# Performance work log

Hardware: AMD Instinct MI355X
Metric: run time of the kernel (lower is better)

The kernel has to match this reference:

```python
import jax, jax.numpy as jnp
import numpy as np

B, K, SD, NA = 2, 512, 60, 5
E, H, D, FF, NL = 256, 4, 64, 1024, 2
EPS_F = 1e-6   # feature_eps in phi(x)=relu(x)+eps
LN_EPS = 1e-5  # torch LayerNorm default eps


def setup_inputs() -> dict:
    key = jax.random.key(0)
    ks = jax.random.split(key, 16)
    f = lambda i, shape, s=0.02: jax.random.normal(ks[i], shape, dtype=jnp.float32) * s
    return {
        "rtg": jax.random.normal(ks[0], (B, K, 1), dtype=jnp.float32),
        "state": jax.random.normal(ks[1], (B, K, SD), dtype=jnp.float32),
        "action": jax.random.normal(ks[2], (B, K, NA), dtype=jnp.float32),
        "rtg_w": f(3, (1, E)), "rtg_b": jnp.zeros((E,), jnp.float32),
        "state_w": f(4, (SD, E)), "state_b": jnp.zeros((E,), jnp.float32),
        "action_w": f(5, (NA, E)), "action_b": jnp.zeros((E,), jnp.float32),
        "pos_emb": f(6, (K, E)),
        "norm1_g": jnp.ones((NL, E), jnp.float32), "norm1_b": jnp.zeros((NL, E), jnp.float32),
        "qkv_w": f(7, (NL, E, 3 * E)), "qkv_b": jnp.zeros((NL, 3 * E), jnp.float32),
        "out_w": f(8, (NL, E, E)), "out_b": jnp.zeros((NL, E), jnp.float32),
        "norm2_g": jnp.ones((NL, E), jnp.float32), "norm2_b": jnp.zeros((NL, E), jnp.float32),
        "ffn1_w": f(9, (NL, E, FF)), "ffn1_b": jnp.zeros((NL, FF), jnp.float32),
        "ffn2_w": f(10, (NL, FF, E)), "ffn2_b": jnp.zeros((NL, E), jnp.float32),
        "normf_g": jnp.ones((E,), jnp.float32), "normf_b": jnp.zeros((E,), jnp.float32),
        "pred_w": f(11, (E, NA)), "pred_b": jnp.zeros((NA,), jnp.float32),
    }


def _ln(x, g, b):
    m = x.mean(-1, keepdims=True)
    v = jnp.mean((x - m) ** 2, -1, keepdims=True)
    return (x - m) * jax.lax.rsqrt(v + LN_EPS) * g + b


def _attn(x, qkv_w, qkv_b, out_w, out_b):
    b, l, _ = x.shape
    qkv = (x @ qkv_w + qkv_b).reshape(b, l, 3, H, D).transpose(2, 0, 3, 1, 4)
    q, k, v = qkv[0], qkv[1], qkv[2]          # each (b,h,l,d)
    q = jax.nn.relu(q) + EPS_F
    k = jax.nn.relu(k) + EPS_F
    kv = jnp.cumsum(jnp.einsum('bhld,bhle->bhlde', k, v), axis=2)  # (b,h,l,d,e)
    kcum = jnp.cumsum(k, axis=2)
    num = jnp.einsum('bhld,bhlde->bhle', q, kv)
    den = jnp.maximum(jnp.einsum('bhld,bhld->bhl', q, kcum)[..., None], 1e-6)
    o = (num / den).transpose(0, 2, 1, 3).reshape(b, l, H * D)
    return o @ out_w + out_b


def reference(rtg, state, action, rtg_w, rtg_b, state_w, state_b, action_w, action_b,
              pos_emb, norm1_g, norm1_b, qkv_w, qkv_b, out_w, out_b,
              norm2_g, norm2_b, ffn1_w, ffn1_b, ffn2_w, ffn2_b,
              normf_g, normf_b, pred_w, pred_b):
    b, k, _ = state.shape
    p = pos_emb[:k][None]
    r = rtg @ rtg_w + rtg_b + p
    s = state @ state_w + state_b + p
    a = action @ action_w + action_b + p
    # interleave (r,s,a) per timestep -> (b, 3k, E)
    x = jnp.stack((r, s, a), axis=2).reshape(b, 3 * k, E)
    for i in range(NL):
        x = x + _attn(_ln(x, norm1_g[i], norm1_b[i]), qkv_w[i], qkv_b[i], out_w[i], out_b[i])
        h = _ln(x, norm2_g[i], norm2_b[i])
        h = jax.nn.gelu(h @ ffn1_w[i] + ffn1_b[i], approximate=False) @ ffn2_w[i] + ffn2_b[i]
        x = x + h
    x = _ln(x, normf_g, normf_b)
    return x[:, 1::3, :] @ pred_w + pred_b  # predict from state tokens -> (b,k,num_actions)
```

## Files before the change

kernel.cpp:

```cpp
#include <hip/hip_runtime.h>
#include <hip/hip_bf16.h>
#include <math.h>

#define B_  2
#define K_  512
#define SD_ 60
#define NA_ 5
#define E_  256
#define H_  4
#define D_  64
#define FF_ 1024
#define NL_ 2
#define L_  (3 * K_)
#define M_  (B_ * L_)
#define EPS_F 1e-6f
#define LN_EPS 1e-5f
#define CHK 64
#define NC_ (L_ / CHK)

using bf16x8 = __attribute__((ext_vector_type(8))) short;
using f32x4  = __attribute__((ext_vector_type(4))) float;
typedef unsigned short u16;

__device__ inline u16 f2b(float v) {
    __hip_bfloat16 h = __float2bfloat16(v);
    return *(u16*)&h;
}
__device__ inline float b2f(u16 v) {
    __hip_bfloat16 h = *(__hip_bfloat16*)&v;
    return __bfloat162float(h);
}

__global__ __launch_bounds__(256) void init_kernel(
    const float* __restrict__ qkv_w, const float* __restrict__ out_w,
    const float* __restrict__ ffn1_w, const float* __restrict__ ffn2_w,
    u16* __restrict__ qkvT, u16* __restrict__ outT,
    u16* __restrict__ f1T, u16* __restrict__ f2T,
    const float* __restrict__ rtg, const float* __restrict__ state,
    const float* __restrict__ action,
    const float* __restrict__ rtg_w, const float* __restrict__ rtg_b,
    const float* __restrict__ state_w, const float* __restrict__ state_b,
    const float* __restrict__ action_w, const float* __restrict__ action_b,
    const float* __restrict__ pos,
    const float* __restrict__ g, const float* __restrict__ bta,
    float* __restrict__ X, u16* __restrict__ Y)
{
    __shared__ u16 T[32][33];
    if (blockIdx.x < 1536) {
        int tb = blockIdx.x;
        int layer = tb / 768;
        int r = tb % 768;
        const float* src; u16* dst; int K, N, tidx;
        if (r < 192)      { src = qkv_w  + layer * 196608; dst = qkvT + layer * 196608; K = 256;  N = 768;  tidx = r; }
        else if (r < 256) { src = out_w  + layer * 65536;  dst = outT + layer * 65536;  K = 256;  N = 256;  tidx = r - 192; }
        else if (r < 512) { src = ffn1_w + layer * 262144; dst = f1T  + layer * 262144; K = 256;  N = 1024; tidx = r - 256; }
        else              { src = ffn2_w + layer * 262144; dst = f2T  + layer * 262144; K = 1024; N = 256;  tidx = r - 512; }
        int tilesN = N >> 5;
        int k0 = (tidx / tilesN) << 5;
        int n0 = (tidx % tilesN) << 5;
        int c = threadIdx.x & 31, r0 = threadIdx.x >> 5;
        for (int rr = r0; rr < 32; rr += 8)
            T[rr][c] = f2b(src[(size_t)(k0 + rr) * N + n0 + c]);
        __syncthreads();
        for (int rr = r0; rr < 32; rr += 8)
            dst[(size_t)(n0 + rr) * K + k0 + c] = T[c][rr];
        return;
    }
    int tok = (blockIdx.x - 1536) * 4 + (threadIdx.x >> 6);
    int lane = threadIdx.x & 63;
    int b = tok / L_, l = tok % L_;
    int j = l % 3, t = l / 3;
    int e0 = lane * 4;
    float4 val = *(const float4*)(pos + t * E_ + e0);
    if (j == 0) {
        float rv = rtg[b * K_ + t];
        float4 w = *(const float4*)(rtg_w + e0);
        float4 bb = *(const float4*)(rtg_b + e0);
        val.x += rv * w.x + bb.x; val.y += rv * w.y + bb.y;
        val.z += rv * w.z + bb.z; val.w += rv * w.w + bb.w;
    } else if (j == 1) {
        float4 a = *(const float4*)(state_b + e0);
        const float* srow = state + ((size_t)b * K_ + t) * SD_;
        for (int i = 0; i < SD_; i++) {
            float s = srow[i];
            float4 w = *(const float4*)(state_w + (size_t)i * E_ + e0);
            a.x += s * w.x; a.y += s * w.y; a.z += s * w.z; a.w += s * w.w;
        }
        val.x += a.x; val.y += a.y; val.z += a.z; val.w += a.w;
    } else {
        float4 a = *(const float4*)(action_b + e0);
        const float* arow = action + ((size_t)b * K_ + t) * NA_;
        #pragma unroll
        for (int i = 0; i < NA_; i++) {
            float s = arow[i];
            float4 w = *(const float4*)(action_w + (size_t)i * E_ + e0);
            a.x += s * w.x; a.y += s * w.y; a.z += s * w.z; a.w += s * w.w;
        }
        val.x += a.x; val.y += a.y; val.z += a.z; val.w += a.w;
    }
    *(float4*)(X + (size_t)tok * E_ + e0) = val;
    float s = val.x + val.y + val.z + val.w;
    #pragma unroll
    for (int o = 32; o; o >>= 1) s += __shfl_xor(s, o, 64);
    float mean = s * (1.f / E_);
    float dx = val.x - mean, dy = val.y - mean, dz = val.z - mean, dw = val.w - mean;
    float q = dx * dx + dy * dy + dz * dz + dw * dw;
    #pragma unroll
    for (int o = 32; o; o >>= 1) q += __shfl_xor(q, o, 64);
    float inv = rsqrtf(q * (1.f / E_) + LN_EPS);
    float4 gv = *(const float4*)(g + e0);
    float4 bv = *(const float4*)(bta + e0);
    ushort4 u;
    u.x = f2b(dx * inv * gv.x + bv.x); u.y = f2b(dy * inv * gv.y + bv.y);
    u.z = f2b(dz * inv * gv.z + bv.z); u.w = f2b(dw * inv * gv.w + bv.w);
    *(ushort4*)(Y + (size_t)tok * E_ + e0) = u;
}

template <int EPI>
__global__ __launch_bounds__(256) void mgemm64(
    const u16* __restrict__ A, const u16* __restrict__ Bt,
    const float* __restrict__ bias,
    u16* __restrict__ C, int M, int N, int Kd)
{
    __shared__ __align__(16) u16 As[2][64 * 40];
    __shared__ __align__(16) u16 Bs[2][128 * 40];
    int tid = threadIdx.x;
    int bm = blockIdx.y * 64, bn = blockIdx.x * 128;
    int wave = tid >> 6, lane = tid & 63;
    int wm = (wave >> 1) * 32, wn = (wave & 1) * 64;
    int lr = lane & 15, kg = lane >> 4;

    int r0 = tid >> 2, g0 = (tid & 3) * 8;

    const u16* Ap  = A  + (size_t)(bm + r0) * Kd + g0;
    const u16* Bp0 = Bt + (size_t)(bn + r0) * Kd + g0;
    const u16* Bp1 = Bt + (size_t)(bn + r0 + 64) * Kd + g0;

    uint4 a0 = *(const uint4*)(Ap);
    uint4 b0 = *(const uint4*)(Bp0);
    uint4 b1 = *(const uint4*)(Bp1);
    *(uint4*)&As[0][r0 * 40 + g0] = a0;
    *(uint4*)&Bs[0][r0 * 40 + g0] = b0;
    *(uint4*)&Bs[0][(r0 + 64) * 40 + g0] = b1;

    f32x4 acc[2][4] = {};
    int NT = Kd >> 5;
    for (int t = 0; t < NT; ++t) {
        int cur = t & 1;
        __syncthreads();
        if (t + 1 < NT) {
            int k1 = (t + 1) << 5;
            a0 = *(const uint4*)(Ap + k1);
            b0 = *(const uint4*)(Bp0 + k1);
            b1 = *(const uint4*)(Bp1 + k1);
        }
        bf16x8 af[2], bg[4];
        #pragma unroll
        for (int i = 0; i < 2; i++)
            af[i] = *(const bf16x8*)&As[cur][(wm + i * 16 + lr) * 40 + kg * 8];
        #pragma unroll
        for (int j = 0; j < 4; j++)
            bg[j] = *(const bf16x8*)&Bs[cur][(wn + j * 16 + lr) * 40 + kg * 8];
        #pragma unroll
        for (int i = 0; i < 2; i++)
            #pragma unroll
            for (int j = 0; j < 4; j++)
                acc[i][j] = __builtin_amdgcn_mfma_f32_16x16x32_bf16(
                    af[i], bg[j], acc[i][j], 0, 0, 0);
        if (t + 1 < NT) {
            *(uint4*)&As[cur ^ 1][r0 * 40 + g0] = a0;
            *(uint4*)&Bs[cur ^ 1][r0 * 40 + g0] = b0;
            *(uint4*)&Bs[cur ^ 1][(r0 + 64) * 40 + g0] = b1;
        }
    }

    #pragma unroll
    for (int i = 0; i < 2; i++) {
        #pragma unroll
        for (int j = 0; j < 4; j++) {
            int col = bn + wn + j * 16 + lr;
            float bc = bias[col];
            #pragma unroll
            for (int r = 0; r < 4; r++) {
                int row = bm + wm + i * 16 + kg * 4 + r;
                float v = acc[i][j][r] + bc;
                if (EPI == 1) v = 0.5f * v * (1.0f + erff(v * 0.70710678118654752f));
                if (EPI == 2) { if (col < 512) v = fmaxf(v, 0.f) + EPS_F; }
                C[(size_t)row * N + col] = f2b(v);
            }
        }
    }
}

template <int LNOUT>
__global__ __launch_bounds__(512) void gres_ln(
    const u16* __restrict__ A, const u16* __restrict__ Bt,
    const float* __restrict__ bias, float* __restrict__ X,
    const float* __restrict__ g, const float* __restrict__ bt,
    u16* __restrict__ Y, int Kd)
{
    __shared__ __align__(16) char smem[5120 + 40960];
    u16* AsB = (u16*)smem;
    u16* BsB = (u16*)(smem + 5120);
    int tid = threadIdx.x;
    int bm = blockIdx.x * 32;
    int wave = tid >> 6, lane = tid & 63;
    int wm = (wave >> 2) * 16;
    int wn = (wave & 3) * 64;
    int lr = lane & 15, kg = lane >> 4;

    int ar = tid >> 2, ag = (tid & 3) * 8;
    bool aload = ar < 32;

    const u16* Ap  = A  + (size_t)(bm + ar) * Kd + ag;
    const u16* Bp0 = Bt + (size_t)(ar) * Kd + ag;
    const u16* Bp1 = Bt + (size_t)(ar + 128) * Kd + ag;

    uint4 a0, b0, b1;
    if (aload) a0 = *(const uint4*)(Ap);
    b0 = *(const uint4*)(Bp0);
    b1 = *(const uint4*)(Bp1);
    if (aload) *(uint4*)&AsB[ar * 40 + ag] = a0;
    *(uint4*)&BsB[ar * 40 + ag] = b0;
    *(uint4*)&BsB[(ar + 128) * 40 + ag] = b1;

    f32x4 acc[4] = {};
    int NT = Kd >> 5;
    for (int t = 0; t < NT; ++t) {
        int cur = t & 1;
        __syncthreads();
        if (t + 1 < NT) {
            int k1 = (t + 1) << 5;
            if (aload) a0 = *(const uint4*)(Ap + k1);
            b0 = *(const uint4*)(Bp0 + k1);
            b1 = *(const uint4*)(Bp1 + k1);
        }
        bf16x8 af = *(const bf16x8*)&AsB[cur * 1280 + (wm + lr) * 40 + kg * 8];
        bf16x8 bg[4];
        #pragma unroll
        for (int j = 0; j < 4; j++)
            bg[j] = *(const bf16x8*)&BsB[cur * 10240 + (wn + j * 16 + lr) * 40 + kg * 8];
        #pragma unroll
        for (int j = 0; j < 4; j++)
            acc[j] = __builtin_amdgcn_mfma_f32_16x16x32_bf16(af, bg[j], acc[j], 0, 0, 0);
        if (t + 1 < NT) {
            if (aload) *(uint4*)&AsB[(cur ^ 1) * 1280 + ar * 40 + ag] = a0;
            *(uint4*)&BsB[(cur ^ 1) * 10240 + ar * 40 + ag] = b0;
            *(uint4*)&BsB[(cur ^ 1) * 10240 + (ar + 128) * 40 + ag] = b1;
        }
    }
    __syncthreads();

    float* Xs = (float*)smem;
    #pragma unroll
    for (int j = 0; j < 4; j++) {
        int col = wn + j * 16 + lr;
        float bc = bias[col];
        #pragma unroll
        for (int rr = 0; rr < 4; rr++) {
            int row = wm + kg * 4 + rr;
            float v = acc[j][rr] + bc + X[(size_t)(bm + row) * 256 + col];
            Xs[row * 260 + col] = v;
        }
    }
    __syncthreads();

    int e0 = lane * 4;
    #pragma unroll
    for (int rq = 0; rq < 4; rq++) {
        int row = wave * 4 + rq;
        float4 v = *(const float4*)&Xs[row * 260 + e0];
        *(float4*)(X + (size_t)(bm + row) * 256 + e0) = v;
        if (LNOUT) {
            float s = v.x + v.y + v.z + v.w;
            #pragma unroll
            for (int o = 32; o; o >>= 1) s += __shfl_xor(s, o, 64);
            float mean = s * (1.f / E_);
            float dx = v.x - mean, dy = v.y - mean, dz = v.z - mean, dw = v.w - mean;
            float q = dx * dx + dy * dy + dz * dz + dw * dw;
            #pragma unroll
            for (int o = 32; o; o >>= 1) q += __shfl_xor(q, o, 64);
            float inv = rsqrtf(q * (1.f / E_) + LN_EPS);
            float4 gv = *(const float4*)(g + e0);
            float4 bv = *(const float4*)(bt + e0);
            ushort4 u;
            u.x = f2b(dx * inv * gv.x + bv.x); u.y = f2b(dy * inv * gv.y + bv.y);
            u.z = f2b(dz * inv * gv.z + bv.z); u.w = f2b(dw * inv * gv.w + bv.w);
            *(ushort4*)(Y + (size_t)(bm + row) * 256 + e0) = u;
        }
    }
}

__global__ __launch_bounds__(256) void chunk_sum_kernel(
    const u16* __restrict__ QKV, float* __restrict__ S, float* __restrict__ Z)
{
    int blk = blockIdx.x;
    int c = blk % NC_;
    int bh = blk / NC_;
    int h = bh % H_;
    int b = bh / H_;
    __shared__ __align__(16) u16 Kt[64 * 72];
    __shared__ __align__(16) u16 Vt[64 * 72];
    int tid = threadIdx.x;
    const size_t base = ((size_t)b * L_ + (size_t)c * CHK) * 768 + h * 64;
    for (int i = tid; i < 1024; i += 256) {
        int t = i >> 4, d4 = (i & 15) << 2;
        ushort4 k = *(const ushort4*)(QKV + base + (size_t)t * 768 + 256 + d4);
        ushort4 v = *(const ushort4*)(QKV + base + (size_t)t * 768 + 512 + d4);
        Kt[(d4 + 0) * 72 + t] = k.x;
        Kt[(d4 + 1) * 72 + t] = k.y;
        Kt[(d4 + 2) * 72 + t] = k.z;
        Kt[(d4 + 3) * 72 + t] = k.w;
        Vt[(d4 + 0) * 72 + t] = v.x;
        Vt[(d4 + 1) * 72 + t] = v.y;
        Vt[(d4 + 2) * 72 + t] = v.z;
        Vt[(d4 + 3) * 72 + t] = v.w;
    }
    __syncthreads();
    int wave = tid >> 6, lane = tid & 63;
    int lr = lane & 15, kg = lane >> 4;
    int wm = wave * 16;
    bf16x8 a0 = *(const bf16x8*)&Kt[(wm + lr) * 72 + kg * 8];
    bf16x8 a1 = *(const bf16x8*)&Kt[(wm + lr) * 72 + 32 + kg * 8];
    f32x4 acc[4] = {};
    #pragma unroll
    for (int j = 0; j < 4; j++) {
        bf16x8 b0 = *(const bf16x8*)&Vt[(j * 16 + lr) * 72 + kg * 8];
        bf16x8 b1 = *(const bf16x8*)&Vt[(j * 16 + lr) * 72 + 32 + kg * 8];
        acc[j] = __builtin_amdgcn_mfma_f32_16x16x32_bf16(a0, b0, acc[j], 0, 0, 0);
        acc[j] = __builtin_amdgcn_mfma_f32_16x16x32_bf16(a1, b1, acc[j], 0, 0, 0);
    }
    if (tid < 64) {
        float z = 0.f;
        #pragma unroll 8
        for (int t = 0; t < 64; t++) z += b2f(Kt[tid * 72 + t]);
        Z[(size_t)blk * 64 + tid] = z;
    }
    float* Sp = S + (size_t)blk * 4096;
    #pragma unroll
    for (int j = 0; j < 4; j++) {
        #pragma unroll
        for (int rr = 0; rr < 4; rr++) {
            int d = wm + kg * 4 + rr;
            int e = j * 16 + lr;
            Sp[d * 64 + e] = acc[j][rr];
        }
    }
}

__global__ __launch_bounds__(256) void chunk_out_kernel(
    const u16* __restrict__ QKV, const float* __restrict__ S,
    const float* __restrict__ Z, u16* __restrict__ O)
{
    int blk = blockIdx.x;
    int c = blk % NC_;
    int bh = blk / NC_;
    int h = bh % H_;
    int b = bh / H_;
    __shared__ __align__(16) u16 Qb[64 * 72];
    __shared__ __align__(16) u16 Kb[64 * 72];
    __shared__ __align__(16) u16 Vt[64 * 72];
    __shared__ __align__(16) u16 KVt[64 * 72];
    __shared__ __align__(16) u16 Ps[64 * 72];
    __shared__ float kzs[64];
    __shared__ float rows[64];
    __shared__ float invs[64];
    int tid = threadIdx.x;
    const size_t base = ((size_t)b * L_ + (size_t)c * CHK) * 768 + h * 64;
    const float* Sbh = S + (size_t)bh * NC_ * 4096;
    for (int i = tid; i < 1024; i += 256) {
        int t = i >> 4, d4 = (i & 15) << 2;
        ushort4 q = *(const ushort4*)(QKV + base + (size_t)t * 768 + d4);
        ushort4 k = *(const ushort4*)(QKV + base + (size_t)t * 768 + 256 + d4);
        ushort4 v = *(const ushort4*)(QKV + base + (size_t)t * 768 + 512 + d4);
        *(ushort4*)&Qb[t * 72 + d4] = q;
        *(ushort4*)&Kb[t * 72 + d4] = k;
        Vt[(d4 + 0) * 72 + t] = v.x;
        Vt[(d4 + 1) * 72 + t] = v.y;
        Vt[(d4 + 2) * 72 + t] = v.z;
        Vt[(d4 + 3) * 72 + t] = v.w;
        int d = t, e4 = d4;
        float4 a = make_float4(0.f, 0.f, 0.f, 0.f);
        for (int cc = 0; cc < c; cc++) {
            float4 s4 = *(const float4*)(Sbh + (size_t)cc * 4096 + d * 64 + e4);
            a.x += s4.x; a.y += s4.y; a.z += s4.z; a.w += s4.w;
        }
        KVt[(e4 + 0) * 72 + d] = f2b(a.x);
        KVt[(e4 + 1) * 72 + d] = f2b(a.y);
        KVt[(e4 + 2) * 72 + d] = f2b(a.z);
        KVt[(e4 + 3) * 72 + d] = f2b(a.w);
    }
    if (tid < 64) {
        float z = 0.f;
        const float* Zbh = Z + (size_t)bh * NC_ * 64;
        for (int cc = 0; cc < c; cc++) z += Zbh[cc * 64 + tid];
        kzs[tid] = z;
    }
    __syncthreads();

    int wave = tid >> 6, lane = tid & 63;
    int lr = lane & 15, kg = lane >> 4;
    int wm = wave * 16;

    bf16x8 aq0 = *(const bf16x8*)&Qb[(wm + lr) * 72 + kg * 8];
    bf16x8 aq1 = *(const bf16x8*)&Qb[(wm + lr) * 72 + 32 + kg * 8];

    f32x4 accs[4] = {};
    #pragma unroll
    for (int j = 0; j < 4; j++) {
        bf16x8 b0 = *(const bf16x8*)&Kb[(j * 16 + lr) * 72 + kg * 8];
        bf16x8 b1 = *(const bf16x8*)&Kb[(j * 16 + lr) * 72 + 32 + kg * 8];
        accs[j] = __builtin_amdgcn_mfma_f32_16x16x32_bf16(aq0, b0, accs[j], 0, 0, 0);
        accs[j] = __builtin_amdgcn_mfma_f32_16x16x32_bf16(aq1, b1, accs[j], 0, 0, 0);
    }
    float rsum[4] = {0.f, 0.f, 0.f, 0.f};
    #pragma unroll
    for (int j = 0; j < 4; j++) {
        #pragma unroll
        for (int rr = 0; rr < 4; rr++) {
            int m = wm + kg * 4 + rr;
            int n = j * 16 + lr;
            float v = (n <= m) ? accs[j][rr] : 0.f;
            rsum[rr] += v;
            Ps[m * 72 + n] = f2b(v);
        }
    }
    #pragma unroll
    for (int rr = 0; rr < 4; rr++) {
        float s = rsum[rr];
        s += __shfl_xor(s, 1, 64);
        s += __shfl_xor(s, 2, 64);
        s += __shfl_xor(s, 4, 64);
        s += __shfl_xor(s, 8, 64);
        if (lr == 0) rows[wm + kg * 4 + rr] = s;
    }
    __syncthreads();

    if (tid < 64) {
        float den = rows[tid];
        float acc = 0.f;
        #pragma unroll 8
        for (int d = 0; d < 64; d++) acc += b2f(Qb[tid * 72 + d]) * kzs[d];
        invs[tid] = 1.f / fmaxf(den + acc, 1e-6f);
    }

    bf16x8 ap0 = *(const bf16x8*)&Ps[(wm + lr) * 72 + kg * 8];
    bf16x8 ap1 = *(const bf16x8*)&Ps[(wm + lr) * 72 + 32 + kg * 8];
    f32x4 accn[4] = {};
    #pragma unroll
    for (int j = 0; j < 4; j++) {
        bf16x8 b0 = *(const bf16x8*)&KVt[(j * 16 + lr) * 72 + kg * 8];
        bf16x8 b1 = *(const bf16x8*)&KVt[(j * 16 + lr) * 72 + 32 + kg * 8];
        accn[j] = __builtin_amdgcn_mfma_f32_16x16x32_bf16(aq0, b0, accn[j], 0, 0, 0);
        accn[j] = __builtin_amdgcn_mfma_f32_16x16x32_bf16(aq1, b1, accn[j], 0, 0, 0);
        bf16x8 c0 = *(const bf16x8*)&Vt[(j * 16 + lr) * 72 + kg * 8];
        bf16x8 c1 = *(const bf16x8*)&Vt[(j * 16 + lr) * 72 + 32 + kg * 8];
        accn[j] = __builtin_amdgcn_mfma_f32_16x16x32_bf16(ap0, c0, accn[j], 0, 0, 0);
        accn[j] = __builtin_amdgcn_mfma_f32_16x16x32_bf16(ap1, c1, accn[j], 0, 0, 0);
    }
    __syncthreads();

    u16* Op = O + ((size_t)b * L_ + (size_t)c * CHK) * E_ + h * 64;
    #pragma unroll
    for (int j = 0; j < 4; j++) {
        #pragma unroll
        for (int rr = 0; rr < 4; rr++) {
            int m = wm + kg * 4 + rr;
            int e = j * 16 + lr;
            Op[(size_t)m * E_ + e] = f2b(accn[j][rr] * invs[m]);
        }
    }
}

__global__ __launch_bounds__(256) void lnpred_kernel(
    const float* __restrict__ X, const float* __restrict__ g,
    const float* __restrict__ bt, const float* __restrict__ W,
    const float* __restrict__ bias, float* __restrict__ Out)
{
    int si = blockIdx.x * 4 + (threadIdx.x >> 6);
    int lane = threadIdx.x & 63;
    int b = si / K_, t = si % K_;
    size_t row = (size_t)b * L_ + 3 * t + 1;
    int e0 = lane * 4;
    float4 v = *(const float4*)(X + row * E_ + e0);
    float s = v.x + v.y + v.z + v.w;
    #pragma unroll
    for (int o = 32; o; o >>= 1) s += __shfl_xor(s, o, 64);
    float mean = s * (1.f / E_);
    float dx = v.x - mean, dy = v.y - mean, dz = v.z - mean, dw = v.w - mean;
    float q = dx * dx + dy * dy + dz * dz + dw * dw;
    #pragma unroll
    for (int o = 32; o; o >>= 1) q += __shfl_xor(q, o, 64);
    float inv = rsqrtf(q * (1.f / E_) + LN_EPS);
    float4 gv = *(const float4*)(g + e0);
    float4 bv = *(const float4*)(bt + e0);
    float y0 = dx * inv * gv.x + bv.x;
    float y1 = dy * inv * gv.y + bv.y;
    float y2 = dz * inv * gv.z + bv.z;
    float y3 = dw * inv * gv.w + bv.w;
    #pragma unroll
    for (int na = 0; na < NA_; na++) {
        float a = y0 * W[(e0 + 0) * NA_ + na] + y1 * W[(e0 + 1) * NA_ + na]
                + y2 * W[(e0 + 2) * NA_ + na] + y3 * W[(e0 + 3) * NA_ + na];
        #pragma unroll
        for (int o = 32; o; o >>= 1) a += __shfl_xor(a, o, 64);
        if (lane == 0) Out[(size_t)si * NA_ + na] = a + bias[na];
    }
}

extern "C" void kernel_launch(void* const* d_in, const int* in_sizes, int n_in,
                              void* d_out, int out_size, void* d_ws, size_t ws_size,
                              hipStream_t stream) {
    const float* rtg      = (const float*)d_in[0];
    const float* state    = (const float*)d_in[1];
    const float* action   = (const float*)d_in[2];
    const float* rtg_w    = (const float*)d_in[3];
    const float* rtg_b    = (const float*)d_in[4];
    const float* state_w  = (const float*)d_in[5];
    const float* state_b  = (const float*)d_in[6];
    const float* action_w = (const float*)d_in[7];
    const float* action_b = (const float*)d_in[8];
    const float* pos_emb  = (const float*)d_in[9];
    const float* norm1_g  = (const float*)d_in[10];
    const float* norm1_b  = (const float*)d_in[11];
    const float* qkv_w    = (const float*)d_in[12];
    const float* qkv_b    = (const float*)d_in[13];
    const float* out_w    = (const float*)d_in[14];
    const float* out_b    = (const float*)d_in[15];
    const float* norm2_g  = (const float*)d_in[16];
    const float* norm2_b  = (const float*)d_in[17];
    const float* ffn1_w   = (const float*)d_in[18];
    const float* ffn1_b   = (const float*)d_in[19];
    const float* ffn2_w   = (const float*)d_in[20];
    const float* ffn2_b   = (const float*)d_in[21];
    const float* normf_g  = (const float*)d_in[22];
    const float* normf_b  = (const float*)d_in[23];
    const float* pred_w   = (const float*)d_in[24];
    const float* pred_b   = (const float*)d_in[25];
    float* out = (float*)d_out;

    float* ws = (float*)d_ws;
    float* x    = ws;
    float* S    = x + 786432;
    float* Z    = S + 786432;
    u16*   yb   = (u16*)(Z + 12288);
    u16*   qkvb = yb + 786432;
    u16*   att  = qkvb + 2359296;
    u16*   h1   = att + 786432;
    u16*   qkvT = h1 + 3145728;
    u16*   outT = qkvT + 393216;
    u16*   f1T  = outT + 131072;
    u16*   f2T  = f1T + 524288;

    init_kernel<<<2304, 256, 0, stream>>>(
        qkv_w, out_w, ffn1_w, ffn2_w, qkvT, outT, f1T, f2T,
        rtg, state, action, rtg_w, rtg_b, state_w, state_b,
        action_w, action_b, pos_emb, norm1_g, norm1_b, x, yb);

    for (int i = 0; i < NL_; i++) {
        mgemm64<2><<<dim3(768 / 128, M_ / 64), 256, 0, stream>>>(
            yb, qkvT + (size_t)i * 196608, qkv_b + i * 768, qkvb,
            M_, 768, E_);
        chunk_sum_kernel<<<B_ * H_ * NC_, 256, 0, stream>>>(qkvb, S, Z);
        chunk_out_kernel<<<B_ * H_ * NC_, 256, 0, stream>>>(qkvb, S, Z, att);
        gres_ln<1><<<M_ / 32, 512, 0, stream>>>(
            att, outT + (size_t)i * 65536, out_b + i * E_, x,
            norm2_g + i * E_, norm2_b + i * E_, yb, E_);
        mgemm64<1><<<dim3(FF_ / 128, M_ / 64), 256, 0, stream>>>(
            yb, f1T + (size_t)i * 262144, ffn1_b + i * FF_, h1,
            M_, FF_, E_);
        if (i == 0)
            gres_ln<1><<<M_ / 32, 512, 0, stream>>>(
                h1, f2T + (size_t)i * 262144, ffn2_b + i * E_, x,
                norm1_g + E_, norm1_b + E_, yb, FF_);
        else
            gres_ln<0><<<M_ / 32, 512, 0, stream>>>(
                h1, f2T + (size_t)i * 262144, ffn2_b + i * E_, x,
                normf_g, normf_b, yb, FF_);
    }
    lnpred_kernel<<<(B_ * K_) / 4, 256, 0, stream>>>(
        x, normf_g, normf_b, pred_w, pred_b, out);
}
```

Measured before the change: 262.5 us.

## Fuse all stages into one persistent kernel with atomic grid barriers

Replaces the sequence of separate kernel launches with a single persistent kernel of 224 blocks. Stages are separated by a software grid barrier built on an atomic counter, and work items are handed out per block in strided loops. It also switches the GEMM tile from 64x128 to 128x128, folds the final LayerNorm and prediction head into the last residual GEMM, and runs the residual GEMM with 256 threads over 32-row tiles. The aim is to remove launch overhead and inter-kernel gaps. The cost is fewer, larger tiles, lower occupancy, and barrier spin time, and the barrier relies on all 224 blocks being resident at once.

```diff
diff --git a/kernel.cpp b/kernel.cpp
--- a/kernel.cpp
+++ b/kernel.cpp
@@ -17,6 +17,7 @@
 #define LN_EPS 1e-5f
 #define CHK 64
 #define NC_ (L_ / CHK)
+#define NBLK 224
 
 using bf16x8 = __attribute__((ext_vector_type(8))) short;
 using f32x4  = __attribute__((ext_vector_type(4))) float;
@@ -31,74 +32,83 @@
     return __bfloat162float(h);
 }
 
-__global__ __launch_bounds__(256) void init_kernel(
-    const float* __restrict__ qkv_w, const float* __restrict__ out_w,
-    const float* __restrict__ ffn1_w, const float* __restrict__ ffn2_w,
-    u16* __restrict__ qkvT, u16* __restrict__ outT,
-    u16* __restrict__ f1T, u16* __restrict__ f2T,
-    const float* __restrict__ rtg, const float* __restrict__ state,
-    const float* __restrict__ action,
-    const float* __restrict__ rtg_w, const float* __restrict__ rtg_b,
-    const float* __restrict__ state_w, const float* __restrict__ state_b,
-    const float* __restrict__ action_w, const float* __restrict__ action_b,
-    const float* __restrict__ pos,
-    const float* __restrict__ g, const float* __restrict__ bta,
-    float* __restrict__ X, u16* __restrict__ Y)
-{
-    __shared__ u16 T[32][33];
-    if (blockIdx.x < 1536) {
-        int tb = blockIdx.x;
-        int layer = tb / 768;
-        int r = tb % 768;
-        const float* src; u16* dst; int K, N, tidx;
-        if (r < 192)      { src = qkv_w  + layer * 196608; dst = qkvT + layer * 196608; K = 256;  N = 768;  tidx = r; }
-        else if (r < 256) { src = out_w  + layer * 65536;  dst = outT + layer * 65536;  K = 256;  N = 256;  tidx = r - 192; }
-        else if (r < 512) { src = ffn1_w + layer * 262144; dst = f1T  + layer * 262144; K = 256;  N = 1024; tidx = r - 256; }
-        else              { src = ffn2_w + layer * 262144; dst = f2T  + layer * 262144; K = 1024; N = 256;  tidx = r - 512; }
-        int tilesN = N >> 5;
-        int k0 = (tidx / tilesN) << 5;
-        int n0 = (tidx % tilesN) << 5;
-        int c = threadIdx.x & 31, r0 = threadIdx.x >> 5;
-        for (int rr = r0; rr < 32; rr += 8)
-            T[rr][c] = f2b(src[(size_t)(k0 + rr) * N + n0 + c]);
-        __syncthreads();
-        for (int rr = r0; rr < 32; rr += 8)
-            dst[(size_t)(n0 + rr) * K + k0 + c] = T[c][rr];
-        return;
-    }
-    int tok = (blockIdx.x - 1536) * 4 + (threadIdx.x >> 6);
+struct MP {
+    const float *rtg, *state, *action, *rtg_w, *rtg_b, *state_w, *state_b,
+                *action_w, *action_b, *pos;
+    const float *n1g, *n1b, *qkv_b, *out_b, *n2g, *n2b, *f1b, *ffn2b,
+                *nfg, *nfb, *pw, *pb;
+    const float *qkv_w, *out_w, *f1w, *f2w;
+    float *x, *S, *Z, *out;
+    u16 *yb, *qkvb, *att, *h1, *qkvT, *outT, *f1T, *f2T;
+    unsigned *bar;
+};
+
+__device__ inline void gbar(unsigned* c) {
+    __syncthreads();
+    if (threadIdx.x == 0) {
+        __threadfence();
+        unsigned t = atomicAdd(c, 1u);
+        unsigned target = (t / gridDim.x + 1u) * gridDim.x;
+        while (atomicAdd(c, 0u) < target) __builtin_amdgcn_s_sleep(2);
+        __threadfence();
+    }
+    __syncthreads();
+}
+
+__device__ void dev_transpose(int tb, const MP& p, char* sm) {
+    u16 (*T)[33] = (u16(*)[33])sm;
+    int layer = tb / 768;
+    int r = tb % 768;
+    const float* src; u16* dst; int K, N, tidx;
+    if (r < 192)      { src = p.qkv_w + layer * 196608; dst = p.qkvT + layer * 196608; K = 256;  N = 768;  tidx = r; }
+    else if (r < 256) { src = p.out_w + layer * 65536;  dst = p.outT + layer * 65536;  K = 256;  N = 256;  tidx = r - 192; }
+    else if (r < 512) { src = p.f1w + layer * 262144;   dst = p.f1T  + layer * 262144; K = 256;  N = 1024; tidx = r - 256; }
+    else              { src = p.f2w + layer * 262144;   dst = p.f2T  + layer * 262144; K = 1024; N = 256;  tidx = r - 512; }
+    int tilesN = N >> 5;
+    int k0 = (tidx / tilesN) << 5;
+    int n0 = (tidx % tilesN) << 5;
+    int c = threadIdx.x & 31, r0 = threadIdx.x >> 5;
+    for (int rr = r0; rr < 32; rr += 8)
+        T[rr][c] = f2b(src[(size_t)(k0 + rr) * N + n0 + c]);
+    __syncthreads();
+    for (int rr = r0; rr < 32; rr += 8)
+        dst[(size_t)(n0 + rr) * K + k0 + c] = T[c][rr];
+}
+
+__device__ void dev_embed(int idx, const MP& p) {
+    int tok = idx * 4 + (threadIdx.x >> 6);
     int lane = threadIdx.x & 63;
     int b = tok / L_, l = tok % L_;
     int j = l % 3, t = l / 3;
     int e0 = lane * 4;
-    float4 val = *(const float4*)(pos + t * E_ + e0);
+    float4 val = *(const float4*)(p.pos + t * E_ + e0);
     if (j == 0) {
-        float rv = rtg[b * K_ + t];
-        float4 w = *(const float4*)(rtg_w + e0);
-        float4 bb = *(const float4*)(rtg_b + e0);
+        float rv = p.rtg[b * K_ + t];
+        float4 w = *(const float4*)(p.rtg_w + e0);
+        float4 bb = *(const float4*)(p.rtg_b + e0);
         val.x += rv * w.x + bb.x; val.y += rv * w.y + bb.y;
         val.z += rv * w.z + bb.z; val.w += rv * w.w + bb.w;
     } else if (j == 1) {
-        float4 a = *(const float4*)(state_b + e0);
-        const float* srow = state + ((size_t)b * K_ + t) * SD_;
+        float4 a = *(const float4*)(p.state_b + e0);
+        const float* srow = p.state + ((size_t)b * K_ + t) * SD_;
         for (int i = 0; i < SD_; i++) {
             float s = srow[i];
-            float4 w = *(const float4*)(state_w + (size_t)i * E_ + e0);
+            float4 w = *(const float4*)(p.state_w + (size_t)i * E_ + e0);
             a.x += s * w.x; a.y += s * w.y; a.z += s * w.z; a.w += s * w.w;
         }
         val.x += a.x; val.y += a.y; val.z += a.z; val.w += a.w;
     } else {
-        float4 a = *(const float4*)(action_b + e0);
-        const float* arow = action + ((size_t)b * K_ + t) * NA_;
+        float4 a = *(const float4*)(p.action_b + e0);
+        const float* arow = p.action + ((size_t)b * K_ + t) * NA_;
         #pragma unroll
         for (int i = 0; i < NA_; i++) {
             float s = arow[i];
-            float4 w = *(const float4*)(action_w + (size_t)i * E_ + e0);
+            float4 w = *(const float4*)(p.action_w + (size_t)i * E_ + e0);
             a.x += s * w.x; a.y += s * w.y; a.z += s * w.z; a.w += s * w.w;
         }
         val.x += a.x; val.y += a.y; val.z += a.z; val.w += a.w;
     }
-    *(float4*)(X + (size_t)tok * E_ + e0) = val;
+    *(float4*)(p.x + (size_t)tok * E_ + e0) = val;
     float s = val.x + val.y + val.z + val.w;
     #pragma unroll
     for (int o = 32; o; o >>= 1) s += __shfl_xor(s, o, 64);
@@ -108,74 +118,82 @@
     #pragma unroll
     for (int o = 32; o; o >>= 1) q += __shfl_xor(q, o, 64);
     float inv = rsqrtf(q * (1.f / E_) + LN_EPS);
-    float4 gv = *(const float4*)(g + e0);
-    float4 bv = *(const float4*)(bta + e0);
+    float4 gv = *(const float4*)(p.n1g + e0);
+    float4 bv = *(const float4*)(p.n1b + e0);
     ushort4 u;
     u.x = f2b(dx * inv * gv.x + bv.x); u.y = f2b(dy * inv * gv.y + bv.y);
     u.z = f2b(dz * inv * gv.z + bv.z); u.w = f2b(dw * inv * gv.w + bv.w);
-    *(ushort4*)(Y + (size_t)tok * E_ + e0) = u;
+    *(ushort4*)(p.yb + (size_t)tok * E_ + e0) = u;
 }
 
 template <int EPI>
-__global__ __launch_bounds__(256) void mgemm64(
+__device__ void dev_mgemm128(
+    int task, int TN,
     const u16* __restrict__ A, const u16* __restrict__ Bt,
-    const float* __restrict__ bias,
-    u16* __restrict__ C, int M, int N, int Kd)
+    const float* __restrict__ bias, u16* __restrict__ C,
+    int N, int Kd, char* sm)
 {
-    __shared__ __align__(16) u16 As[2][64 * 40];
-    __shared__ __align__(16) u16 Bs[2][128 * 40];
+    u16* As = (u16*)sm;
+    u16* Bs = (u16*)(sm + 20480);
     int tid = threadIdx.x;
-    int bm = blockIdx.y * 64, bn = blockIdx.x * 128;
+    int bm = (task / TN) * 128, bn = (task % TN) * 128;
     int wave = tid >> 6, lane = tid & 63;
-    int wm = (wave >> 1) * 32, wn = (wave & 1) * 64;
+    int wm = (wave >> 1) * 64, wn = (wave & 1) * 64;
     int lr = lane & 15, kg = lane >> 4;
 
     int r0 = tid >> 2, g0 = (tid & 3) * 8;
-
-    const u16* Ap  = A  + (size_t)(bm + r0) * Kd + g0;
+    int r1 = r0 + 64;
+
+    const u16* Ap0 = A + (size_t)(bm + r0) * Kd + g0;
+    const u16* Ap1 = A + (size_t)(bm + r1) * Kd + g0;
     const u16* Bp0 = Bt + (size_t)(bn + r0) * Kd + g0;
-    const u16* Bp1 = Bt + (size_t)(bn + r0 + 64) * Kd + g0;
-
-    uint4 a0 = *(const uint4*)(Ap);
+    const u16* Bp1 = Bt + (size_t)(bn + r1) * Kd + g0;
+
+    uint4 a0 = *(const uint4*)(Ap0);
+    uint4 a1 = *(const uint4*)(Ap1);
     uint4 b0 = *(const uint4*)(Bp0);
     uint4 b1 = *(const uint4*)(Bp1);
-    *(uint4*)&As[0][r0 * 40 + g0] = a0;
-    *(uint4*)&Bs[0][r0 * 40 + g0] = b0;
-    *(uint4*)&Bs[0][(r0 + 64) * 40 + g0] = b1;
-
-    f32x4 acc[2][4] = {};
+    *(uint4*)&As[r0 * 40 + g0] = a0;
+    *(uint4*)&As[r1 * 40 + g0] = a1;
+    *(uint4*)&Bs[r0 * 40 + g0] = b0;
+    *(uint4*)&Bs[r1 * 40 + g0] = b1;
+
+    f32x4 acc[4][4] = {};
     int NT = Kd >> 5;
     for (int t = 0; t < NT; ++t) {
         int cur = t & 1;
         __syncthreads();
         if (t + 1 < NT) {
             int k1 = (t + 1) << 5;
-            a0 = *(const uint4*)(Ap + k1);
+            a0 = *(const uint4*)(Ap0 + k1);
+            a1 = *(const uint4*)(Ap1 + k1);
             b0 = *(const uint4*)(Bp0 + k1);
             b1 = *(const uint4*)(Bp1 + k1);
         }
-        bf16x8 af[2], bg[4];
-        #pragma unroll
-        for (int i = 0; i < 2; i++)
-            af[i] = *(const bf16x8*)&As[cur][(wm + i * 16 + lr) * 40 + kg * 8];
+        bf16x8 af[4], bg[4];
+        #pragma unroll
+        for (int i = 0; i < 4; i++)
+            af[i] = *(const bf16x8*)&As[cur * 5120 + (wm + i * 16 + lr) * 40 + kg * 8];
         #pragma unroll
         for (int j = 0; j < 4; j++)
-            bg[j] = *(const bf16x8*)&Bs[cur][(wn + j * 16 + lr) * 40 + kg * 8];
-        #pragma unroll
-        for (int i = 0; i < 2; i++)
+            bg[j] = *(const bf16x8*)&Bs[cur * 5120 + (wn + j * 16 + lr) * 40 + kg * 8];
+        #pragma unroll
+        for (int i = 0; i < 4; i++)
             #pragma unroll
             for (int j = 0; j < 4; j++)
                 acc[i][j] = __builtin_amdgcn_mfma_f32_16x16x32_bf16(
                     af[i], bg[j], acc[i][j], 0, 0, 0);
         if (t + 1 < NT) {
-            *(uint4*)&As[cur ^ 1][r0 * 40 + g0] = a0;
-            *(uint4*)&Bs[cur ^ 1][r0 * 40 + g0] = b0;
-            *(uint4*)&Bs[cur ^ 1][(r0 + 64) * 40 + g0] = b1;
-        }
-    }
-
-    #pragma unroll
-    for (int i = 0; i < 2; i++) {
+            *(uint4*)&As[(cur ^ 1) * 5120 + r0 * 40 + g0] = a0;
+            *(uint4*)&As[(cur ^ 1) * 5120 + r1 * 40 + g0] = a1;
+            *(uint4*)&Bs[(cur ^ 1) * 5120 + r0 * 40 + g0] = b0;
+            *(uint4*)&Bs[(cur ^ 1) * 5120 + r1 * 40 + g0] = b1;
+        }
+    }
+    __syncthreads();
+
+    #pragma unroll
+    for (int i = 0; i < 4; i++) {
         #pragma unroll
         for (int j = 0; j < 4; j++) {
             int col = bn + wn + j * 16 + lr;
@@ -192,115 +210,15 @@
     }
 }
 
-template <int LNOUT>
-__global__ __launch_bounds__(512) void gres_ln(
-    const u16* __restrict__ A, const u16* __restrict__ Bt,
-    const float* __restrict__ bias, float* __restrict__ X,
-    const float* __restrict__ g, const float* __restrict__ bt,
-    u16* __restrict__ Y, int Kd)
-{
-    __shared__ __align__(16) char smem[5120 + 40960];
-    u16* AsB = (u16*)smem;
-    u16* BsB = (u16*)(smem + 5120);
-    int tid = threadIdx.x;
-    int bm = blockIdx.x * 32;
-    int wave = tid >> 6, lane = tid & 63;
-    int wm = (wave >> 2) * 16;
-    int wn = (wave & 3) * 64;
-    int lr = lane & 15, kg = lane >> 4;
-
-    int ar = tid >> 2, ag = (tid & 3) * 8;
-    bool aload = ar < 32;
-
-    const u16* Ap  = A  + (size_t)(bm + ar) * Kd + ag;
-    const u16* Bp0 = Bt + (size_t)(ar) * Kd + ag;
-    const u16* Bp1 = Bt + (size_t)(ar + 128) * Kd + ag;
-
-    uint4 a0, b0, b1;
-    if (aload) a0 = *(const uint4*)(Ap);
-    b0 = *(const uint4*)(Bp0);
-    b1 = *(const uint4*)(Bp1);
-    if (aload) *(uint4*)&AsB[ar * 40 + ag] = a0;
-    *(uint4*)&BsB[ar * 40 + ag] = b0;
-    *(uint4*)&BsB[(ar + 128) * 40 + ag] = b1;
-
-    f32x4 acc[4] = {};
-    int NT = Kd >> 5;
-    for (int t = 0; t < NT; ++t) {
-        int cur = t & 1;
-        __syncthreads();
-        if (t + 1 < NT) {
-            int k1 = (t + 1) << 5;
-            if (aload) a0 = *(const uint4*)(Ap + k1);
-            b0 = *(const uint4*)(Bp0 + k1);
-            b1 = *(const uint4*)(Bp1 + k1);
-        }
-        bf16x8 af = *(const bf16x8*)&AsB[cur * 1280 + (wm + lr) * 40 + kg * 8];
-        bf16x8 bg[4];
-        #pragma unroll
-        for (int j = 0; j < 4; j++)
-            bg[j] = *(const bf16x8*)&BsB[cur * 10240 + (wn + j * 16 + lr) * 40 + kg * 8];
-        #pragma unroll
-        for (int j = 0; j < 4; j++)
-            acc[j] = __builtin_amdgcn_mfma_f32_16x16x32_bf16(af, bg[j], acc[j], 0, 0, 0);
-        if (t + 1 < NT) {
-            if (aload) *(uint4*)&AsB[(cur ^ 1) * 1280 + ar * 40 + ag] = a0;
-            *(uint4*)&BsB[(cur ^ 1) * 10240 + ar * 40 + ag] = b0;
-            *(uint4*)&BsB[(cur ^ 1) * 10240 + (ar + 128) * 40 + ag] = b1;
-        }
-    }
-    __syncthreads();
-
-    float* Xs = (float*)smem;
-    #pragma unroll
-    for (int j = 0; j < 4; j++) {
-        int col = wn + j * 16 + lr;
-        float bc = bias[col];
-        #pragma unroll
-        for (int rr = 0; rr < 4; rr++) {
-            int row = wm + kg * 4 + rr;
-            float v = acc[j][rr] + bc + X[(size_t)(bm + row) * 256 + col];
-            Xs[row * 260 + col] = v;
-        }
-    }
-    __syncthreads();
-
-    int e0 = lane * 4;
-    #pragma unroll
-    for (int rq = 0; rq < 4; rq++) {
-        int row = wave * 4 + rq;
-        float4 v = *(const float4*)&Xs[row * 260 + e0];
-        *(float4*)(X + (size_t)(bm + row) * 256 + e0) = v;
-        if (LNOUT) {
-            float s = v.x + v.y + v.z + v.w;
-            #pragma unroll
-            for (int o = 32; o; o >>= 1) s += __shfl_xor(s, o, 64);
-            float mean = s * (1.f / E_);
-            float dx = v.x - mean, dy = v.y - mean, dz = v.z - mean, dw = v.w - mean;
-            float q = dx * dx + dy * dy + dz * dz + dw * dw;
-            #pragma unroll
-            for (int o = 32; o; o >>= 1) q += __shfl_xor(q, o, 64);
-            float inv = rsqrtf(q * (1.f / E_) + LN_EPS);
-            float4 gv = *(const float4*)(g + e0);
-            float4 bv = *(const float4*)(bt + e0);
-            ushort4 u;
-            u.x = f2b(dx * inv * gv.x + bv.x); u.y = f2b(dy * inv * gv.y + bv.y);
-            u.z = f2b(dz * inv * gv.z + bv.z); u.w = f2b(dw * inv * gv.w + bv.w);
-            *(ushort4*)(Y + (size_t)(bm + row) * 256 + e0) = u;
-        }
-    }
-}
-
-__global__ __launch_bounds__(256) void chunk_sum_kernel(
-    const u16* __restrict__ QKV, float* __restrict__ S, float* __restrict__ Z)
-{
-    int blk = blockIdx.x;
+__device__ void dev_chunk_sum(int blk, const u16* __restrict__ QKV,
+                              float* __restrict__ S, float* __restrict__ Z,
+                              char* sm) {
     int c = blk % NC_;
     int bh = blk / NC_;
     int h = bh % H_;
     int b = bh / H_;
-    __shared__ __align__(16) u16 Kt[64 * 72];
-    __shared__ __align__(16) u16 Vt[64 * 72];
+    u16* Kt = (u16*)sm;
+    u16* Vt = (u16*)(sm + 9216);
     int tid = threadIdx.x;
     const size_t base = ((size_t)b * L_ + (size_t)c * CHK) * 768 + h * 64;
     for (int i = tid; i < 1024; i += 256) {
@@ -348,23 +266,22 @@
     }
 }
 
-__global__ __launch_bounds__(256) void chunk_out_kernel(
-    const u16* __restrict__ QKV, const float* __restrict__ S,
-    const float* __restrict__ Z, u16* __restrict__ O)
-{
-    int blk = blockIdx.x;
+__device__ void dev_chunk_out(int blk, const u16* __restrict__ QKV,
+                              const float* __restrict__ S,
+                              const float* __restrict__ Z,
+                              u16* __restrict__ O, char* sm) {
     int c = blk % NC_;
     int bh = blk / NC_;
     int h = bh % H_;
     int b = bh / H_;
-    __shared__ __align__(16) u16 Qb[64 * 72];
-    __shared__ __align__(16) u16 Kb[64 * 72];
-    __shared__ __align__(16) u16 Vt[64 * 72];
-    __shared__ __align__(16) u16 KVt[64 * 72];
-    __shared__ __align__(16) u16 Ps[64 * 72];
-    __shared__ float kzs[64];
-    __shared__ float rows[64];
-    __shared__ float invs[64];
+    u16* Qb  = (u16*)sm;
+    u16* Kb  = (u16*)(sm + 9216);
+    u16* Vt  = (u16*)(sm + 18432);
+    u16* KVt = (u16*)(sm + 27648);
+    u16* Ps  = (u16*)(sm + 36864);
+    float* kzs  = (float*)(sm + 46080);
+    float* rows = kzs + 64;
+    float* invs = rows + 64;
     int tid = threadIdx.x;
     const size_t base = ((size_t)b * L_ + (size_t)c * CHK) * 768 + h * 64;
     const float* Sbh = S + (size_t)bh * NC_ * 4096;
@@ -472,73 +389,206 @@
     }
 }
 
-__global__ __launch_bounds__(256) void lnpred_kernel(
-    const float* __restrict__ X, const float* __restrict__ g,
-    const float* __restrict__ bt, const float* __restrict__ W,
-    const float* __restrict__ bias, float* __restrict__ Out)
+template <int MODE>
+__device__ void dev_gres32(
+    int task, const u16* __restrict__ A, const u16* __restrict__ Bt,
+    const float* __restrict__ bias, float* __restrict__ X,
+    const float* __restrict__ g, const float* __restrict__ bt,
+    u16* __restrict__ Y, const float* __restrict__ W,
+    const float* __restrict__ pb, float* __restrict__ Out,
+    int Kd, char* sm)
 {
-    int si = blockIdx.x * 4 + (threadIdx.x >> 6);
-    int lane = threadIdx.x & 63;
-    int b = si / K_, t = si % K_;
-    size_t row = (size_t)b * L_ + 3 * t + 1;
+    u16* AsB = (u16*)sm;
+    u16* BsB = (u16*)(sm + 5120);
+    int tid = threadIdx.x;
+    int bm = task * 32;
+    int wave = tid >> 6, lane = tid & 63;
+    int wn = wave * 64;
+    int lr = lane & 15, kg = lane >> 4;
+
+    int sr = tid >> 2, ag = (tid & 3) * 8;
+    bool al = sr < 32;
+
+    const u16* Ap = A + (size_t)(bm + sr) * Kd + ag;
+    const u16* Bp = Bt + (size_t)sr * Kd + ag;
+
+    uint4 aR, bR[4];
+    if (al) aR = *(const uint4*)(Ap);
+    #pragma unroll
+    for (int q = 0; q < 4; q++) bR[q] = *(const uint4*)(Bp + (size_t)(64 * q) * Kd);
+    if (al) *(uint4*)&AsB[sr * 40 + ag] = aR;
+    #pragma unroll
+    for (int q = 0; q < 4; q++) *(uint4*)&BsB[(sr + 64 * q) * 40 + ag] = bR[q];
+
+    f32x4 acc[2][4] = {};
+    int NT = Kd >> 5;
+    for (int t = 0; t < NT; ++t) {
+        int cur = t & 1;
+        __syncthreads();
+        if (t + 1 < NT) {
+            int k1 = (t + 1) << 5;
+            if (al) aR = *(const uint4*)(Ap + k1);
+            #pragma unroll
+            for (int q = 0; q < 4; q++)
+                bR[q] = *(const uint4*)(Bp + (size_t)(64 * q) * Kd + k1);
+        }
+        bf16x8 af[2], bg[4];
+        #pragma unroll
+        for (int i = 0; i < 2; i++)
+            af[i] = *(const bf16x8*)&AsB[cur * 1280 + (i * 16 + lr) * 40 + kg * 8];
+        #pragma unroll
+        for (int j = 0; j < 4; j++)
+            bg[j] = *(const bf16x8*)&BsB[cur * 10240 + (wn + j * 16 + lr) * 40 + kg * 8];
+        #pragma unroll
+        for (int i = 0; i < 2; i++)
+            #pragma unroll
+            for (int j = 0; j < 4; j++)
+                acc[i][j] = __builtin_amdgcn_mfma_f32_16x16x32_bf16(
+                    af[i], bg[j], acc[i][j], 0, 0, 0);
+        if (t + 1 < NT) {
+            if (al) *(uint4*)&AsB[(cur ^ 1) * 1280 + sr * 40 + ag] = aR;
+            #pragma unroll
+            for (int q = 0; q < 4; q++)
+                *(uint4*)&BsB[(cur ^ 1) * 10240 + (sr + 64 * q) * 40 + ag] = bR[q];
+        }
+    }
+    __syncthreads();
+
+    float* Xs = (float*)sm;
+    #pragma unroll
+    for (int i = 0; i < 2; i++) {
+        #pragma unroll
+        for (int j = 0; j < 4; j++) {
+            int col = wn + j * 16 + lr;
+            float bc = bias[col];
+            #pragma unroll
+            for (int rr = 0; rr < 4; rr++) {
+                int row = i * 16 + kg * 4 + rr;
+                float v = acc[i][j][rr] + bc + X[(size_t)(bm + row) * 256 + col];
+                Xs[row * 260 + col] = v;
+            }
+        }
+    }
+    __syncthreads();
+
     int e0 = lane * 4;
-    float4 v = *(const float4*)(X + row * E_ + e0);
-    float s = v.x + v.y + v.z + v.w;
-    #pragma unroll
-    for (int o = 32; o; o >>= 1) s += __shfl_xor(s, o, 64);
-    float mean = s * (1.f / E_);
-    float dx = v.x - mean, dy = v.y - mean, dz = v.z - mean, dw = v.w - mean;
-    float q = dx * dx + dy * dy + dz * dz + dw * dw;
-    #pragma unroll
-    for (int o = 32; o; o >>= 1) q += __shfl_xor(q, o, 64);
-    float inv = rsqrtf(q * (1.f / E_) + LN_EPS);
-    float4 gv = *(const float4*)(g + e0);
-    float4 bv = *(const float4*)(bt + e0);
-    float y0 = dx * inv * gv.x + bv.x;
-    float y1 = dy * inv * gv.y + bv.y;
-    float y2 = dz * inv * gv.z + bv.z;
-    float y3 = dw * inv * gv.w + bv.w;
-    #pragma unroll
-    for (int na = 0; na < NA_; na++) {
-        float a = y0 * W[(e0 + 0) * NA_ + na] + y1 * W[(e0 + 1) * NA_ + na]
-                + y2 * W[(e0 + 2) * NA_ + na] + y3 * W[(e0 + 3) * NA_ + na];
-        #pragma unroll
-        for (int o = 32; o; o >>= 1) a += __shfl_xor(a, o, 64);
-        if (lane == 0) Out[(size_t)si * NA_ + na] = a + bias[na];
+    #pragma unroll
+    for (int rq = 0; rq < 8; rq++) {
+        int row = wave * 8 + rq;
+        float4 v = *(const float4*)&Xs[row * 260 + e0];
+        if (MODE == 1) {
+            *(float4*)(X + (size_t)(bm + row) * 256 + e0) = v;
+            float s = v.x + v.y + v.z + v.w;
+            #pragma unroll
+            for (int o = 32; o; o >>= 1) s += __shfl_xor(s, o, 64);
+            float mean = s * (1.f / E_);
+            float dx = v.x - mean, dy = v.y - mean, dz = v.z - mean, dw = v.w - mean;
+            float q = dx * dx + dy * dy + dz * dz + dw * dw;
+            #pragma unroll
+            for (int o = 32; o; o >>= 1) q += __shfl_xor(q, o, 64);
+            float inv = rsqrtf(q * (1.f / E_) + LN_EPS);
+            float4 gv = *(const float4*)(g + e0);
+            float4 bv = *(const float4*)(bt + e0);
+            ushort4 u;
+            u.x = f2b(dx * inv * gv.x + bv.x); u.y = f2b(dy * inv * gv.y + bv.y);
+            u.z = f2b(dz * inv * gv.z + bv.z); u.w = f2b(dw * inv * gv.w + bv.w);
+            *(ushort4*)(Y + (size_t)(bm + row) * 256 + e0) = u;
+        } else {
+            int gr = bm + row;
+            int b = gr / L_, l = gr % L_;
+            if (l % 3 == 1) {
+                float s = v.x + v.y + v.z + v.w;
+                #pragma unroll
+                for (int o = 32; o; o >>= 1) s += __shfl_xor(s, o, 64);
+                float mean = s * (1.f / E_);
+                float dx = v.x - mean, dy = v.y - mean, dz = v.z - mean, dw = v.w - mean;
+                float q = dx * dx + dy * dy + dz * dz + dw * dw;
+                #pragma unroll
+                for (int o = 32; o; o >>= 1) q += __shfl_xor(q, o, 64);
+                float inv = rsqrtf(q * (1.f / E_) + LN_EPS);
+                float4 gv = *(const float4*)(g + e0);
+                float4 bv = *(const float4*)(bt + e0);
+                float y0 = dx * inv * gv.x + bv.x;
+                float y1 = dy * inv * gv.y + bv.y;
+                float y2 = dz * inv * gv.z + bv.z;
+                float y3 = dw * inv * gv.w + bv.w;
+                int si = b * K_ + l / 3;
+                #pragma unroll
+                for (int na = 0; na < NA_; na++) {
+                    float a = y0 * W[(e0 + 0) * NA_ + na] + y1 * W[(e0 + 1) * NA_ + na]
+                            + y2 * W[(e0 + 2) * NA_ + na] + y3 * W[(e0 + 3) * NA_ + na];
+                    #pragma unroll
+                    for (int o = 32; o; o >>= 1) a += __shfl_xor(a, o, 64);
+                    if (lane == 0) Out[(size_t)si * NA_ + na] = a + pb[na];
+                }
+            }
+        }
+    }
+}
+
+__global__ __launch_bounds__(256) void mega(MP p) {
+    __shared__ __align__(16) char sm[46848];
+    int NB = gridDim.x;
+
+    for (int t = blockIdx.x; t < 2304; t += NB) {
+        if (t < 1536) dev_transpose(t, p, sm);
+        else dev_embed(t - 1536, p);
+        __syncthreads();
+    }
+    gbar(p.bar);
+
+    for (int i = 0; i < NL_; i++) {
+        for (int t = blockIdx.x; t < 144; t += NB) {
+            dev_mgemm128<2>(t, 6, p.yb, p.qkvT + (size_t)i * 196608,
+                            p.qkv_b + i * 768, p.qkvb, 768, 256, sm);
+            __syncthreads();
+        }
+        gbar(p.bar);
+        for (int t = blockIdx.x; t < 192; t += NB) {
+            dev_chunk_sum(t, p.qkvb, p.S, p.Z, sm);
+            __syncthreads();
+        }
+        gbar(p.bar);
+        for (int t = blockIdx.x; t < 192; t += NB) {
+            dev_chunk_out(t, p.qkvb, p.S, p.Z, p.att, sm);
+            __syncthreads();
+        }
+        gbar(p.bar);
+        for (int t = blockIdx.x; t < 96; t += NB) {
+            dev_gres32<1>(t, p.att, p.outT + (size_t)i * 65536, p.out_b + i * E_,
+                          p.x, p.n2g + i * E_, p.n2b + i * E_, p.yb,
+                          nullptr, nullptr, nullptr, 256, sm);
+            __syncthreads();
+        }
+        gbar(p.bar);
+        for (int t = blockIdx.x; t < 192; t += NB) {
+            dev_mgemm128<1>(t, 8, p.yb, p.f1T + (size_t)i * 262144,
+                            p.f1b + i * FF_, p.h1, 1024, 256, sm);
+            __syncthreads();
+        }
+        gbar(p.bar);
+        if (i == 0) {
+            for (int t = blockIdx.x; t < 96; t += NB) {
+                dev_gres32<1>(t, p.h1, p.f2T, p.ffn2b, p.x,
+                              p.n1g + E_, p.n1b + E_, p.yb,
+                              nullptr, nullptr, nullptr, 1024, sm);
+                __syncthreads();
+            }
+            gbar(p.bar);
+        } else {
+            for (int t = blockIdx.x; t < 96; t += NB) {
+                dev_gres32<2>(t, p.h1, p.f2T + (size_t)i * 262144, p.ffn2b + i * E_,
+                              p.x, p.nfg, p.nfb, nullptr,
+                              p.pw, p.pb, p.out, 1024, sm);
+                __syncthreads();
+            }
+        }
     }
 }
 
 extern "C" void kernel_launch(void* const* d_in, const int* in_sizes, int n_in,
                               void* d_out, int out_size, void* d_ws, size_t ws_size,
                               hipStream_t stream) {
-    const float* rtg      = (const float*)d_in[0];
-    const float* state    = (const float*)d_in[1];
-    const float* action   = (const float*)d_in[2];
-    const float* rtg_w    = (const float*)d_in[3];
-    const float* rtg_b    = (const float*)d_in[4];
-    const float* state_w  = (const float*)d_in[5];
-    const float* state_b  = (const float*)d_in[6];
-    const float* action_w = (const float*)d_in[7];
-    const float* action_b = (const float*)d_in[8];
-    const float* pos_emb  = (const float*)d_in[9];
-    const float* norm1_g  = (const float*)d_in[10];
-    const float* norm1_b  = (const float*)d_in[11];
-    const float* qkv_w    = (const float*)d_in[12];
-    const float* qkv_b    = (const float*)d_in[13];
-    const float* out_w    = (const float*)d_in[14];
-    const float* out_b    = (const float*)d_in[15];
-    const float* norm2_g  = (const float*)d_in[16];
-    const float* norm2_b  = (const float*)d_in[17];
-    const float* ffn1_w   = (const float*)d_in[18];
-    const float* ffn1_b   = (const float*)d_in[19];
-    const float* ffn2_w   = (const float*)d_in[20];
-    const float* ffn2_b   = (const float*)d_in[21];
-    const float* normf_g  = (const float*)d_in[22];
-    const float* normf_b  = (const float*)d_in[23];
-    const float* pred_w   = (const float*)d_in[24];
-    const float* pred_b   = (const float*)d_in[25];
-    float* out = (float*)d_out;
-
     float* ws = (float*)d_ws;
     float* x    = ws;
     float* S    = x + 786432;
@@ -551,33 +601,41 @@
     u16*   outT = qkvT + 393216;
     u16*   f1T  = outT + 131072;
     u16*   f2T  = f1T + 524288;
-
-    init_kernel<<<2304, 256, 0, stream>>>(
-        qkv_w, out_w, ffn1_w, ffn2_w, qkvT, outT, f1T, f2T,
-        rtg, state, action, rtg_w, rtg_b, state_w, state_b,
-        action_w, action_b, pos_emb, norm1_g, norm1_b, x, yb);
-
-    for (int i = 0; i < NL_; i++) {
-        mgemm64<2><<<dim3(768 / 128, M_ / 64), 256, 0, stream>>>(
-            yb, qkvT + (size_t)i * 196608, qkv_b + i * 768, qkvb,
-            M_, 768, E_);
-        chunk_sum_kernel<<<B_ * H_ * NC_, 256, 0, stream>>>(qkvb, S, Z);
-        chunk_out_kernel<<<B_ * H_ * NC_, 256, 0, stream>>>(qkvb, S, Z, att);
-        gres_ln<1><<<M_ / 32, 512, 0, stream>>>(
-            att, outT + (size_t)i * 65536, out_b + i * E_, x,
-            norm2_g + i * E_, norm2_b + i * E_, yb, E_);
-        mgemm64<1><<<dim3(FF_ / 128, M_ / 64), 256, 0, stream>>>(
-            yb, f1T + (size_t)i * 262144, ffn1_b + i * FF_, h1,
-            M_, FF_, E_);
-        if (i == 0)
-            gres_ln<1><<<M_ / 32, 512, 0, stream>>>(
-                h1, f2T + (size_t)i * 262144, ffn2_b + i * E_, x,
-                norm1_g + E_, norm1_b + E_, yb, FF_);
-        else
-            gres_ln<0><<<M_ / 32, 512, 0, stream>>>(
-                h1, f2T + (size_t)i * 262144, ffn2_b + i * E_, x,
-                normf_g, normf_b, yb, FF_);
-    }
-    lnpred_kernel<<<(B_ * K_) / 4, 256, 0, stream>>>(
-        x, normf_g, normf_b, pred_w, pred_b, out);
-}
+    unsigned* bar = (unsigned*)(f2T + 524288);
+
+    hipMemsetAsync(bar, 0, 64, stream);
+
+    MP p;
+    p.rtg      = (const float*)d_in[0];
+    p.state    = (const float*)d_in[1];
+    p.action   = (const float*)d_in[2];
+    p.rtg_w    = (const float*)d_in[3];
+    p.rtg_b    = (const float*)d_in[4];
+    p.state_w  = (const float*)d_in[5];
+    p.state_b  = (const float*)d_in[6];
+    p.action_w = (const float*)d_in[7];
+    p.action_b = (const float*)d_in[8];
+    p.pos      = (const float*)d_in[9];
+    p.n1g      = (const float*)d_in[10];
+    p.n1b      = (const float*)d_in[11];
+    p.qkv_w    = (const float*)d_in[12];
+    p.qkv_b    = (const float*)d_in[13];
+    p.out_w    = (const float*)d_in[14];
+    p.out_b    = (const float*)d_in[15];
+    p.n2g      = (const float*)d_in[16];
+    p.n2b      = (const float*)d_in[17];
+    p.f1w      = (const float*)d_in[18];
+    p.f1b      = (const float*)d_in[19];
+    p.f2w      = (const float*)d_in[20];
+    p.ffn2b    = (const float*)d_in[21];
+    p.nfg      = (const float*)d_in[22];
+    p.nfb      = (const float*)d_in[23];
+    p.pw       = (const float*)d_in[24];
+    p.pb       = (const float*)d_in[25];
+    p.x = x; p.S = S; p.Z = Z; p.out = (float*)d_out;
+    p.yb = yb; p.qkvb = qkvb; p.att = att; p.h1 = h1;
+    p.qkvT = qkvT; p.outT = outT; p.f1T = f1T; p.f2T = f2T;
+    p.bar = bar;
+
+    mega<<<dim3(NBLK), dim3(256), 0, stream>>>(p);
+}
```

After: 573.9 us. 2.19x slower.
